# Kernel tuning notes

Measured on AMD Instinct MI355X. Metric: run time of the kernel, lower is better.

Reference implementation:

```python
import jax, jax.numpy as jnp
import numpy as np

# Static per-expert capacities (tokens are laid out contiguously per expert)
CAPS = [1024, 512, 1024, 256, 1024, 512, 128, 1024, 512, 1024, 256, 512, 1024, 128, 64, 512]
TOTAL = sum(CAPS)  # 9536
E, H, I = 16, 1024, 4096
OFFSETS = np.concatenate([[0], np.cumsum(CAPS)])


def setup_inputs() -> dict:
    key = jax.random.key(0)
    ks = jax.random.split(key, 5)
    x = jax.random.normal(ks[0], (TOTAL, H), dtype=jnp.float32)
    W1 = jax.random.normal(ks[1], (E, I, H), dtype=jnp.float32) * 0.02
    b1 = jax.random.normal(ks[2], (E, I), dtype=jnp.float32) * 0.02
    W2 = jax.random.normal(ks[3], (E, H, I), dtype=jnp.float32) * 0.02
    b2 = jax.random.normal(ks[4], (E, H), dtype=jnp.float32) * 0.02
    return {"x": x, "W1": W1, "b1": b1, "W2": W2, "b2": b2}


def reference(x, W1, b1, W2, b2):
    # Grouped GEMM FFN: expert e processes rows [OFFSETS[e]:OFFSETS[e+1]]
    # out = gelu(x_e @ W1[e].T + b1[e]) @ W2[e].T + b2[e]
    outs = []
    for e in range(E):  # fixed, static loop over experts (capacities are static)
        xs = x[OFFSETS[e]:OFFSETS[e + 1]]                      # [cap_e, H]
        h = jax.nn.gelu(xs @ W1[e].T + b1[e], approximate=False)  # [cap_e, I]
        outs.append(h @ W2[e].T + b2[e])                       # [cap_e, H]
    return jnp.concatenate(outs, axis=0)                       # [TOTAL, H]
```

## Files before the change

### kernel.cpp

```cpp
#include <hip/hip_runtime.h>
#include <math.h>

typedef __attribute__((ext_vector_type(8))) short short8;
typedef __attribute__((ext_vector_type(4))) float f32x4;
typedef __attribute__((ext_vector_type(2))) unsigned int u32x2;
typedef __attribute__((ext_vector_type(4))) unsigned int u32x4;

#define E_NUM 16
constexpr int CAPS[E_NUM] = {1024,512,1024,256,1024,512,128,1024,512,1024,256,512,1024,128,64,512};
constexpr int OFFS[E_NUM] = {0,1024,1536,2560,2816,3840,4352,4480,5504,6016,7040,7296,7808,8832,8960,9024};
constexpr int cdiv_(int a, int b){ return (a + b - 1) / b; }
constexpr int ilog2_(int v){ int l = 0; while ((1 << l) < v) ++l; return l; }

__device__ __forceinline__ unsigned int cvt_pk_bf16(float a, float b){
  unsigned int r;
  asm("v_cvt_pk_bf16_f32 %0, %1, %2" : "=v"(r) : "v"(a), "v"(b));
  return r;
}

typedef __attribute__((address_space(1))) const unsigned char gas_u8;
typedef __attribute__((address_space(3))) unsigned char las_u8;
__device__ __forceinline__ void gl_lds16(const void* g, void* l){
  __builtin_amdgcn_global_load_lds((gas_u8*)g, (las_u8*)l, 16, 0, 0);
}

__global__ __launch_bounds__(256) void cvt_bf16_kernel(const float* __restrict__ x,
                                                       unsigned short* __restrict__ xb, int n8)
{
  int i = blockIdx.x * blockDim.x + threadIdx.x;
  const int stride = gridDim.x * blockDim.x;
  for (; i < n8; i += stride) {
    f32x4 a = *reinterpret_cast<const f32x4*>(x + (size_t)i * 8);
    f32x4 b = *reinterpret_cast<const f32x4*>(x + (size_t)i * 8 + 4);
    u32x2 lo, hi;
    lo[0] = cvt_pk_bf16(a[0], a[1]); lo[1] = cvt_pk_bf16(a[2], a[3]);
    hi[0] = cvt_pk_bf16(b[0], b[1]); hi[1] = cvt_pk_bf16(b[2], b[3]);
    *reinterpret_cast<u32x2*>(xb + (size_t)i * 8)     = lo;
    *reinterpret_cast<u32x2*>(xb + (size_t)i * 8 + 4) = hi;
  }
}

template<bool A_BF16, int NDIM, int KDIM, int LOG_GN, int NWG>
__global__ __launch_bounds__(512, 2)
void g1_gemm256(const void* __restrict__ Av, const float* __restrict__ W,
                const float* __restrict__ bias, void* __restrict__ Outv)
{
  constexpr int A_BYTES = 256 * 64;
  constexpr int B_BYTES = 256 * 128;
  constexpr int BUF  = A_BYTES + B_BYTES;
  constexpr int NBUF = A_BF16 ? 3 : 2;
  constexpr int GN   = 1 << LOG_GN;
  constexpr int NTT  = KDIM / 32;
  static_assert(NWG % 8 == 0);
  static_assert(NTT >= 3);

  __shared__ __align__(16) char smem[NBUF * BUF];

  const int tid  = threadIdx.x;
  const int braw = blockIdx.x;
  const int tt = (braw & 7) * (NWG / 8) + (braw >> 3);

  int m0 = 0, n0 = 0, Me = 0, tok0 = 0;
  size_t wbase = 0, bbase = 0;
  {
    int acc0 = 0;
    #pragma unroll
    for (int i = 0; i < E_NUM; ++i) {
      const int mt  = cdiv_(CAPS[i], 256);
      const int lmt = ilog2_(mt);
      const int nb  = mt * (NDIM / 256);
      if (tt >= acc0 && tt < acc0 + nb) {
        const int loc = tt - acc0;
        const int g   = loc >> (lmt + LOG_GN);
        const int rem = loc & ((mt << LOG_GN) - 1);
        m0   = (rem >> LOG_GN) * 256;
        n0   = ((g << LOG_GN) | (rem & (GN - 1))) * 256;
        Me   = CAPS[i];
        tok0 = OFFS[i];
        wbase = (size_t)i * NDIM * KDIM;
        bbase = (size_t)i * NDIM;
      }
      acc0 += nb;
    }
  }
  const float* Wb = W + wbase;

  const int lane = tid & 63;
  const int wv   = tid >> 6;

  const unsigned short* Ah = (const unsigned short*)Av;
  const float*          Af = (const float*)Av;

  auto stageA = [&](int buf, int kt) {
    const unsigned short* Ag = Ah + (size_t)(tok0 + m0) * KDIM + kt * 32;
    char* dst0 = smem + buf * BUF;
    #pragma unroll
    for (int j = 0; j < 2; ++j) {
      const int rbase = j * 128 + wv * 16;
      const int r     = rbase + (lane >> 2);
      const int blk   = (lane & 3) ^ (r & 3);
      gl_lds16((const void*)(Ag + (size_t)r * KDIM + blk * 8), (void*)(dst0 + rbase * 64));
    }
  };
  auto stageB = [&](int buf, int kt) {
    const float* Bg = Wb + (size_t)n0 * KDIM + kt * 32;
    char* dst0 = smem + buf * BUF + A_BYTES;
    #pragma unroll
    for (int j = 0; j < 4; ++j) {
      const int rbase = j * 64 + wv * 8;
      const int r     = rbase + (lane >> 3);
      const int blk   = (lane & 7) ^ (r & 7);
      gl_lds16((const void*)(Bg + (size_t)r * KDIM + blk * 4), (void*)(dst0 + rbase * 128));
    }
  };

  const int fr = tid >> 1;
  const int fcq = (tid & 1) * 2;
  f32x4 raf[4];
  auto loadA_reg = [&](int kt) {
    const float* Ap = Af + (size_t)(tok0 + m0 + fr) * KDIM + kt * 32 + fcq * 8;
    #pragma unroll
    for (int i = 0; i < 4; ++i) raf[i] = *reinterpret_cast<const f32x4*>(Ap + i * 4);
  };
  auto writeA_reg = [&](int buf) {
    char* ab = smem + buf * BUF;
    #pragma unroll
    for (int i = 0; i < 2; ++i) {
      u32x2 p;
      p[0] = cvt_pk_bf16(raf[2*i][0], raf[2*i][1]);
      p[1] = cvt_pk_bf16(raf[2*i][2], raf[2*i][3]);
      const int blk = (fcq + i) ^ (fr & 3);
      *reinterpret_cast<u32x2*>(ab + fr * 64 + blk * 16) = p;
    }
  };

  const int wm   = (wv >> 2) * 128;
  const int wn   = (wv & 3) * 64;
  const int lrow = lane & 15;
  const int pa0  = (((lane >> 4) ^ (lane & 3)) << 4);
  const int pb0  = ((((lane >> 4) << 1) ^ (lane & 7)) << 4);

  f32x4 acc_[8][4];
  #pragma unroll
  for (int i = 0; i < 8; ++i)
    #pragma unroll
    for (int j = 0; j < 4; ++j)
      acc_[i][j] = (f32x4){0.f, 0.f, 0.f, 0.f};

  auto compute = [&](int cur) {
    const char* ab  = smem + cur * BUF;
    const char* bbp = smem + cur * BUF + A_BYTES;
    short8 bfr[4];
    #pragma unroll
    for (int f = 0; f < 4; ++f) {
      const char* rowp = bbp + (size_t)(wn + f * 16 + lrow) * 128;
      f32x4 lo = *reinterpret_cast<const f32x4*>(rowp + pb0);
      f32x4 hi = *reinterpret_cast<const f32x4*>(rowp + (pb0 ^ 16));
      u32x4 pk;
      pk[0] = cvt_pk_bf16(lo[0], lo[1]); pk[1] = cvt_pk_bf16(lo[2], lo[3]);
      pk[2] = cvt_pk_bf16(hi[0], hi[1]); pk[3] = cvt_pk_bf16(hi[2], hi[3]);
      bfr[f] = __builtin_bit_cast(short8, pk);
    }
    #pragma unroll
    for (int i = 0; i < 8; ++i) {
      short8 afr = *reinterpret_cast<const short8*>(ab + (wm + i * 16 + lrow) * 64 + pa0);
      #pragma unroll
      for (int j = 0; j < 4; ++j)
        acc_[i][j] = __builtin_amdgcn_mfma_f32_16x16x32_bf16(afr, bfr[j], acc_[i][j], 0, 0, 0);
    }
  };

  if constexpr (A_BF16) {
    stageA(0, 0); stageB(0, 0);
    stageA(1, 1); stageB(1, 1);
    int cur = 0, nx2 = 2;
    for (int kt = 0; kt < NTT; ++kt) {
      if (kt + 1 < NTT) asm volatile("s_waitcnt vmcnt(6)\n\ts_barrier" ::: "memory");
      else              asm volatile("s_waitcnt vmcnt(0)\n\ts_barrier" ::: "memory");
      __builtin_amdgcn_sched_barrier(0);
      if (kt + 2 < NTT) { stageA(nx2, kt + 2); stageB(nx2, kt + 2); }
      compute(cur);
      cur = (cur == 2) ? 0 : cur + 1;
      nx2 = (nx2 == 2) ? 0 : nx2 + 1;
    }
  } else {
    loadA_reg(0); stageB(0, 0); writeA_reg(0);
    __syncthreads();
    for (int kt = 0; kt < NTT; ++kt) {
      const int cur = kt & 1;
      if (kt + 1 < NTT) { stageB(cur ^ 1, kt + 1); loadA_reg(kt + 1); }
      compute(cur);
      if (kt + 1 < NTT) writeA_reg(cur ^ 1);
      __syncthreads();
    }
  }

  float bv[4];
  #pragma unroll
  for (int f = 0; f < 4; ++f)
    bv[f] = bias[bbase + n0 + wn + f * 16 + lrow];

  unsigned short* Oh = (unsigned short*)Outv;
  if constexpr (A_BF16) {
    __syncthreads();
    unsigned short* hout = (unsigned short*)smem;
    #pragma unroll
    for (int i = 0; i < 8; ++i) {
      const int rbase = wm + i * 16 + (lane >> 4) * 4;
      #pragma unroll
      for (int j = 0; j < 4; ++j) {
        #pragma unroll
        for (int jj = 0; jj < 4; ++jj) {
          float xv = acc_[i][j][jj] + bv[j];
          float y2 = xv * (1.5957691216057308f + 0.07135481627f * xv * xv);
          float g  = xv * __builtin_amdgcn_rcpf(1.0f + __expf(-y2));
          hout[(rbase + jj) * 256 + wn + j * 16 + lrow] = (unsigned short)(cvt_pk_bf16(g, g) & 0xFFFFu);
        }
      }
    }
    __syncthreads();
    #pragma unroll
    for (int s = 0; s < 16; ++s) {
      const int row = s * 16 + (tid >> 5);
      const int c   = (tid & 31) * 8;
      if (m0 + row < Me) {
        *reinterpret_cast<short8*>(Oh + (size_t)(tok0 + m0 + row) * NDIM + n0 + c)
          = *reinterpret_cast<const short8*>(hout + row * 256 + c);
      }
    }
  } else {
    #pragma unroll
    for (int i = 0; i < 8; ++i) {
      const int rbase = wm + i * 16 + (lane >> 4) * 4;
      #pragma unroll
      for (int j = 0; j < 4; ++j) {
        #pragma unroll
        for (int jj = 0; jj < 4; ++jj) {
          int grow = m0 + rbase + jj;
          if (grow < Me) {
            float xv = acc_[i][j][jj] + bv[j];
            float y2 = xv * (1.5957691216057308f + 0.07135481627f * xv * xv);
            float g  = xv * __builtin_amdgcn_rcpf(1.0f + __expf(-y2));
            Oh[(size_t)(tok0 + grow) * NDIM + n0 + wn + j * 16 + lrow]
              = (unsigned short)(cvt_pk_bf16(g, g) & 0xFFFFu);
          }
        }
      }
    }
  }
}

template<int NDIM, int KDIM, int LOG_GN, int NWG, int KS>
__global__ __launch_bounds__(256, 8)
void g2_gemm128(const unsigned short* __restrict__ Ah, const float* __restrict__ W,
                const float* __restrict__ bias, float* __restrict__ Of)
{
  constexpr int A_BYTES = 128 * 64;
  constexpr int B_BYTES = 128 * 64;
  constexpr int GN   = 1 << LOG_GN;
  constexpr int NT   = KDIM / (KS * 32);
  constexpr int NWG1 = NWG / KS;
  static_assert(NWG % 8 == 0);

  __shared__ __align__(16) char smem[2 * A_BYTES + 2 * B_BYTES];

  const int tid  = threadIdx.x;
  const int braw = blockIdx.x;
  const int t = (braw & 7) * (NWG / 8) + (braw >> 3);

  const int kc    = t / NWG1;
  const int tt    = t % NWG1;
  const int kbase = kc * (KDIM / KS);

  int m0 = 0, n0 = 0, Me = 0, tok0 = 0;
  size_t wbase = 0, bbase = 0;
  {
    int acc0 = 0;
    #pragma unroll
    for (int i = 0; i < E_NUM; ++i) {
      const int mt  = cdiv_(CAPS[i], 128);
      const int lmt = ilog2_(mt);
      const int nb  = mt * (NDIM / 128);
      if (tt >= acc0 && tt < acc0 + nb) {
        const int loc = tt - acc0;
        const int g   = loc >> (lmt + LOG_GN);
        const int rem = loc & ((mt << LOG_GN) - 1);
        m0   = (rem >> LOG_GN) * 128;
        n0   = ((g << LOG_GN) | (rem & (GN - 1))) * 128;
        Me   = CAPS[i];
        tok0 = OFFS[i];
        wbase = (size_t)i * NDIM * KDIM;
        bbase = (size_t)i * NDIM;
      }
      acc0 += nb;
    }
  }
  const float* Wb = W + wbase;

  const int lane = tid & 63;
  const int wv   = tid >> 6;
  const int sr   = tid >> 3;
  const int sc   = (tid & 7) * 8;
  const int spc  = sc ^ (((sr >> 2) & 3) << 4);

  f32x4 rb[4];
  auto loadB = [&](int kt) {
    const int k0 = kbase + kt * 32;
    #pragma unroll
    for (int i = 0; i < 4; ++i)
      rb[i] = *reinterpret_cast<const f32x4*>(Wb + (size_t)(n0 + sr + 32 * i) * KDIM + k0 + (sc >> 1));
  };
  auto writeB = [&](int buf) {
    char* bb = smem + 2 * A_BYTES + buf * B_BYTES;
    #pragma unroll
    for (int i = 0; i < 4; ++i) {
      u32x2 p;
      p[0] = cvt_pk_bf16(rb[i][0], rb[i][1]);
      p[1] = cvt_pk_bf16(rb[i][2], rb[i][3]);
      *reinterpret_cast<u32x2*>(bb + (sr + 32 * i) * 64 + spc) = p;
    }
  };

  auto stageA = [&](int buf, int kt) {
    const unsigned short* Ag = Ah + (size_t)(tok0 + m0) * KDIM + kbase + kt * 32;
    char* dst0 = smem + buf * A_BYTES;
    #pragma unroll
    for (int j = 0; j < 2; ++j) {
      const int rbase = wv * 32 + j * 16;
      const int r     = rbase + (lane >> 2);
      const int blk   = (lane & 3) ^ ((r >> 2) & 3);
      gl_lds16((const void*)(Ag + (size_t)r * KDIM + blk * 8), (void*)(dst0 + rbase * 64));
    }
  };

  const int wm   = (wv >> 1) * 64;
  const int wn   = (wv & 1) * 64;
  const int lrow = lane & 15;
  const int fcs  = ((lane >> 4) << 4) ^ (((lane >> 2) & 3) << 4);

  f32x4 acc_[4][4];
  #pragma unroll
  for (int i = 0; i < 4; ++i)
    #pragma unroll
    for (int j = 0; j < 4; ++j)
      acc_[i][j] = (f32x4){0.f, 0.f, 0.f, 0.f};

  auto mfma_step = [&](int cur) {
    const char* ab = smem + cur * A_BYTES;
    const char* bb = smem + 2 * A_BYTES + cur * B_BYTES;
    short8 afr[4], bfr[4];
    #pragma unroll
    for (int f = 0; f < 4; ++f)
      afr[f] = *reinterpret_cast<const short8*>(ab + (wm + f * 16 + lrow) * 64 + fcs);
    #pragma unroll
    for (int f = 0; f < 4; ++f)
      bfr[f] = *reinterpret_cast<const short8*>(bb + (wn + f * 16 + lrow) * 64 + fcs);
    #pragma unroll
    for (int i = 0; i < 4; ++i)
      #pragma unroll
      for (int j = 0; j < 4; ++j)
        acc_[i][j] = __builtin_amdgcn_mfma_f32_16x16x32_bf16(afr[i], bfr[j], acc_[i][j], 0, 0, 0);
  };

  loadB(0); stageA(0, 0); writeB(0);
  __syncthreads();

  for (int kt = 0; kt < NT; ++kt) {
    const int cur = kt & 1;
    if (kt + 1 < NT) { loadB(kt + 1); stageA(cur ^ 1, kt + 1); }
    mfma_step(cur);
    if (kt + 1 < NT) writeB(cur ^ 1);
    __syncthreads();
  }

  float bv[4];
  #pragma unroll
  for (int f = 0; f < 4; ++f)
    bv[f] = bias[bbase + n0 + wn + f * 16 + lrow];

  constexpr float BS = 1.0f / (float)KS;
  #pragma unroll
  for (int i = 0; i < 4; ++i) {
    const int rbase = wm + i * 16 + (lane >> 4) * 4;
    #pragma unroll
    for (int jj = 0; jj < 4; ++jj) {
      int grow = m0 + rbase + jj;
      if (grow < Me) {
        #pragma unroll
        for (int j = 0; j < 4; ++j) {
          float v = acc_[i][j][jj] + bv[j] * BS;
          float* p = Of + (size_t)(tok0 + grow) * NDIM + n0 + wn + j * 16 + lrow;
          if constexpr (KS > 1) unsafeAtomicAdd(p, v);
          else                  *p = v;
        }
      }
    }
  }
}

extern "C" void kernel_launch(void* const* d_in, const int* in_sizes, int n_in,
                              void* d_out, int out_size, void* d_ws, size_t ws_size,
                              hipStream_t stream)
{
  const float* x  = (const float*)d_in[0];
  const float* W1 = (const float*)d_in[1];
  const float* b1 = (const float*)d_in[2];
  const float* W2 = (const float*)d_in[3];
  const float* b2 = (const float*)d_in[4];
  float* out = (float*)d_out;

  constexpr size_t H_BYTES  = (size_t)9536 * 4096 * 2;
  constexpr size_t XB_BYTES = (size_t)9536 * 1024 * 2;
  unsigned short* h  = (unsigned short*)d_ws;
  unsigned short* xb = (unsigned short*)((char*)d_ws + H_BYTES);

  const bool use_xb = ws_size >= H_BYTES + XB_BYTES;

  hipMemsetAsync(d_out, 0, (size_t)out_size * sizeof(float), stream);

  if (use_xb) {
    cvt_bf16_kernel<<<2048, 256, 0, stream>>>(x, xb, 9536 * 1024 / 8);
    g1_gemm256<true, 4096, 1024, 2, 624>
        <<<624, 512, 0, stream>>>((const void*)xb, W1, b1, (void*)h);
  } else {
    g1_gemm256<false, 4096, 1024, 2, 624>
        <<<624, 512, 0, stream>>>((const void*)x, W1, b1, (void*)h);
  }

  g2_gemm128<1024, 4096, 2, 1200, 2>
      <<<1200, 256, 0, stream>>>(h, W2, b2, out);
}
```

Measured before the change: 368.5 us.

## Stage fp32 W2 tiles directly to LDS with triple-buffered async pipeline

The second GEMM now loads W2 fp32 tiles straight into LDS with global_load_lds instead of going through registers and converting before the LDS write. The bf16 conversion moves to fragment-read time. A three-stage ring buffer with manual vmcnt waits and barriers keeps two tiles in flight. LDS use grows from 32KB to 72KB, so launch bounds drop to 4 blocks per CU, and each B tile is now converted by several waves instead of once.

Measured after the change: 364.4 us. No clear change (-1.1%).

```diff
diff --git a/kernel.cpp b/kernel.cpp
--- a/kernel.cpp
+++ b/kernel.cpp
@@ -251,18 +251,20 @@
 }
 
 template<int NDIM, int KDIM, int LOG_GN, int NWG, int KS>
-__global__ __launch_bounds__(256, 8)
+__global__ __launch_bounds__(256, 4)
 void g2_gemm128(const unsigned short* __restrict__ Ah, const float* __restrict__ W,
                 const float* __restrict__ bias, float* __restrict__ Of)
 {
   constexpr int A_BYTES = 128 * 64;
-  constexpr int B_BYTES = 128 * 64;
+  constexpr int B_BYTES = 128 * 128;
+  constexpr int BUF  = A_BYTES + B_BYTES;
   constexpr int GN   = 1 << LOG_GN;
   constexpr int NT   = KDIM / (KS * 32);
   constexpr int NWG1 = NWG / KS;
   static_assert(NWG % 8 == 0);
-
-  __shared__ __align__(16) char smem[2 * A_BYTES + 2 * B_BYTES];
+  static_assert(NT >= 3);
+
+  __shared__ __align__(16) char smem[3 * BUF];
 
   const int tid  = threadIdx.x;
   const int braw = blockIdx.x;
@@ -299,44 +301,35 @@
 
   const int lane = tid & 63;
   const int wv   = tid >> 6;
-  const int sr   = tid >> 3;
-  const int sc   = (tid & 7) * 8;
-  const int spc  = sc ^ (((sr >> 2) & 3) << 4);
-
-  f32x4 rb[4];
-  auto loadB = [&](int kt) {
-    const int k0 = kbase + kt * 32;
-    #pragma unroll
-    for (int i = 0; i < 4; ++i)
-      rb[i] = *reinterpret_cast<const f32x4*>(Wb + (size_t)(n0 + sr + 32 * i) * KDIM + k0 + (sc >> 1));
-  };
-  auto writeB = [&](int buf) {
-    char* bb = smem + 2 * A_BYTES + buf * B_BYTES;
-    #pragma unroll
-    for (int i = 0; i < 4; ++i) {
-      u32x2 p;
-      p[0] = cvt_pk_bf16(rb[i][0], rb[i][1]);
-      p[1] = cvt_pk_bf16(rb[i][2], rb[i][3]);
-      *reinterpret_cast<u32x2*>(bb + (sr + 32 * i) * 64 + spc) = p;
-    }
-  };
 
   auto stageA = [&](int buf, int kt) {
     const unsigned short* Ag = Ah + (size_t)(tok0 + m0) * KDIM + kbase + kt * 32;
-    char* dst0 = smem + buf * A_BYTES;
+    char* dst0 = smem + buf * BUF;
     #pragma unroll
     for (int j = 0; j < 2; ++j) {
-      const int rbase = wv * 32 + j * 16;
+      const int rbase = j * 64 + wv * 16;
       const int r     = rbase + (lane >> 2);
-      const int blk   = (lane & 3) ^ ((r >> 2) & 3);
+      const int blk   = (lane & 3) ^ (r & 3);
       gl_lds16((const void*)(Ag + (size_t)r * KDIM + blk * 8), (void*)(dst0 + rbase * 64));
+    }
+  };
+  auto stageB = [&](int buf, int kt) {
+    const float* Bg = Wb + (size_t)n0 * KDIM + kbase + kt * 32;
+    char* dst0 = smem + buf * BUF + A_BYTES;
+    #pragma unroll
+    for (int j = 0; j < 4; ++j) {
+      const int rbase = j * 32 + wv * 8;
+      const int r     = rbase + (lane >> 3);
+      const int blk   = (lane & 7) ^ (r & 7);
+      gl_lds16((const void*)(Bg + (size_t)r * KDIM + blk * 4), (void*)(dst0 + rbase * 128));
     }
   };
 
   const int wm   = (wv >> 1) * 64;
   const int wn   = (wv & 1) * 64;
   const int lrow = lane & 15;
-  const int fcs  = ((lane >> 4) << 4) ^ (((lane >> 2) & 3) << 4);
+  const int pa0  = (((lane >> 4) ^ (lane & 3)) << 4);
+  const int pb0  = ((((lane >> 4) << 1) ^ (lane & 7)) << 4);
 
   f32x4 acc_[4][4];
   #pragma unroll
@@ -345,32 +338,40 @@
     for (int j = 0; j < 4; ++j)
       acc_[i][j] = (f32x4){0.f, 0.f, 0.f, 0.f};
 
-  auto mfma_step = [&](int cur) {
-    const char* ab = smem + cur * A_BYTES;
-    const char* bb = smem + 2 * A_BYTES + cur * B_BYTES;
-    short8 afr[4], bfr[4];
-    #pragma unroll
-    for (int f = 0; f < 4; ++f)
-      afr[f] = *reinterpret_cast<const short8*>(ab + (wm + f * 16 + lrow) * 64 + fcs);
-    #pragma unroll
-    for (int f = 0; f < 4; ++f)
-      bfr[f] = *reinterpret_cast<const short8*>(bb + (wn + f * 16 + lrow) * 64 + fcs);
-    #pragma unroll
-    for (int i = 0; i < 4; ++i)
+  auto compute = [&](int cur) {
+    const char* ab  = smem + cur * BUF;
+    const char* bbp = smem + cur * BUF + A_BYTES;
+    short8 bfr[4];
+    #pragma unroll
+    for (int f = 0; f < 4; ++f) {
+      const char* rowp = bbp + (size_t)(wn + f * 16 + lrow) * 128;
+      f32x4 lo = *reinterpret_cast<const f32x4*>(rowp + pb0);
+      f32x4 hi = *reinterpret_cast<const f32x4*>(rowp + (pb0 ^ 16));
+      u32x4 pk;
+      pk[0] = cvt_pk_bf16(lo[0], lo[1]); pk[1] = cvt_pk_bf16(lo[2], lo[3]);
+      pk[2] = cvt_pk_bf16(hi[0], hi[1]); pk[3] = cvt_pk_bf16(hi[2], hi[3]);
+      bfr[f] = __builtin_bit_cast(short8, pk);
+    }
+    #pragma unroll
+    for (int i = 0; i < 4; ++i) {
+      short8 afr = *reinterpret_cast<const short8*>(ab + (wm + i * 16 + lrow) * 64 + pa0);
       #pragma unroll
       for (int j = 0; j < 4; ++j)
-        acc_[i][j] = __builtin_amdgcn_mfma_f32_16x16x32_bf16(afr[i], bfr[j], acc_[i][j], 0, 0, 0);
-  };
-
-  loadB(0); stageA(0, 0); writeB(0);
-  __syncthreads();
-
+        acc_[i][j] = __builtin_amdgcn_mfma_f32_16x16x32_bf16(afr, bfr[j], acc_[i][j], 0, 0, 0);
+    }
+  };
+
+  stageA(0, 0); stageB(0, 0);
+  stageA(1, 1); stageB(1, 1);
+  int cur = 0, nx2 = 2;
   for (int kt = 0; kt < NT; ++kt) {
-    const int cur = kt & 1;
-    if (kt + 1 < NT) { loadB(kt + 1); stageA(cur ^ 1, kt + 1); }
-    mfma_step(cur);
-    if (kt + 1 < NT) writeB(cur ^ 1);
-    __syncthreads();
+    if (kt + 1 < NT) asm volatile("s_waitcnt vmcnt(6)\n\ts_barrier" ::: "memory");
+    else             asm volatile("s_waitcnt vmcnt(0)\n\ts_barrier" ::: "memory");
+    __builtin_amdgcn_sched_barrier(0);
+    if (kt + 2 < NT) { stageA(nx2, kt + 2); stageB(nx2, kt + 2); }
+    compute(cur);
+    cur = (cur == 2) ? 0 : cur + 1;
+    nx2 = (nx2 == 2) ? 0 : nx2 + 1;
   }
 
   float bv[4];
```
